# Performance work log

Measured on AMD Instinct MI355X. Metric: run time of the kernel, lower is better.

## Reference

```python
import jax, jax.numpy as jnp
import numpy as np

B, N, NCTX, DIM, H, DH, NMEM = 2, 1024, 2048, 1024, 16, 64, 16


def setup_inputs() -> dict:
    key = jax.random.key(0)
    ks = jax.random.split(key, 24)
    r = lambda i, shape, s=1.0: jax.random.normal(ks[i], shape, dtype=jnp.float32) * s
    w = 0.02  # linear weight scale
    return {
        "x": r(0, (B, N, DIM)),
        "context": r(1, (2, B, NCTX, DIM)),
        "wq1": r(2, (DIM, H * DH), w), "wk1": r(3, (DIM, H * DH), w), "wv1": r(4, (DIM, H * DH), w),
        "wq2": r(5, (DIM, H * DH), w), "wk2": r(6, (DIM, H * DH), w), "wv2": r(7, (DIM, H * DH), w),
        "th_pre1": r(8, (H, H), 0.25), "th_post1": r(9, (H, H), 0.25),
        "th_pre2": r(10, (H, H), 0.25), "th_post2": r(11, (H, H), 0.25),
        "scale1": jnp.full((1, H, 1, 1), -3.0, jnp.float32) + r(12, (1, H, 1, 1), 0.05),
        "scale2": jnp.full((1, H, 1, 1), -3.0, jnp.float32) + r(13, (1, H, 1, 1), 0.05),
        "mem_k1": r(14, (H, NMEM, DH)), "mem_v1": r(15, (H, NMEM, DH)),
        "mem_k2": r(16, (H, NMEM, DH)), "mem_v2": r(17, (H, NMEM, DH)),
        "hs1": jnp.ones((1, H, 1, 1), jnp.float32) + r(18, (1, H, 1, 1), 0.05),
        "hs2": jnp.ones((1, H, 1, 1), jnp.float32) + r(19, (1, H, 1, 1), 0.05),
        "wo1": r(20, (H * DH, DIM), w), "wo2": r(21, (H * DH, DIM), w),
    }


def _l2norm(t):
    # F.normalize: t / max(||t||, eps)
    n = jnp.linalg.norm(t, axis=-1, keepdims=True)
    return t / jnp.maximum(n, 1e-12)


def _split_heads(t, b):
    # [b, n, h*d] -> [b, h, n, d]
    return t.reshape(b, -1, H, DH).transpose(0, 2, 1, 3)


def _attend(x, kv, wq, wk, wv, th_pre, th_post, scale_p, mem_k, mem_v, hs, wo):
    b, n, _ = x.shape
    q = _split_heads(x @ wq, b)    # [b,h,n,d]
    k = _split_heads(kv @ wk, b)   # [b,h,j,d]
    v = _split_heads(kv @ wv, b)
    # memory key/values prepended
    k = jnp.concatenate([jnp.broadcast_to(mem_k[None], (b, H, NMEM, DH)), k], axis=2)
    v = jnp.concatenate([jnp.broadcast_to(mem_v[None], (b, H, NMEM, DH)), v], axis=2)
    # qk-norm with learned per-head temperature: scale = 1 / clamp(exp(p), min=0.01)
    q, k = _l2norm(q), _l2norm(k)
    scale = 1.0 / jnp.maximum(jnp.exp(scale_p), 0.01)
    dots = jnp.einsum('bhid,bhjd->bhij', q, k) * scale
    # talking heads: 1x1 Conv2d over head channel == head-mixing matmul
    dots = jnp.einsum('gh,bhij->bgij', th_pre, dots)
    attn = jax.nn.softmax(dots, axis=-1)
    attn = jnp.einsum('gh,bhij->bgij', th_post, attn)
    out = jnp.einsum('bhij,bhjd->bhid', attn, v) * hs  # head_scale
    out = out.transpose(0, 2, 1, 3).reshape(b, n, H * DH)
    return out @ wo


def reference(x, context, wq1, wk1, wv1, wq2, wk2, wv2,
              th_pre1, th_post1, th_pre2, th_post2,
              scale1, scale2, mem_k1, mem_v1, mem_k2, mem_v2,
              hs1, hs2, wo1, wo2):
    o1 = _attend(x, context[0], wq1, wk1, wv1, th_pre1, th_post1, scale1, mem_k1, mem_v1, hs1, wo1)
    o2 = _attend(x, context[1], wq2, wk2, wv2, th_pre2, th_post2, scale2, mem_k2, mem_v2, hs2, wo2)
    return o1 + o2
```

## Files before the change

### kernel.cpp

```cpp
#include <hip/hip_runtime.h>
#include <hip/hip_bf16.h>

#define Bb    2
#define Nn    1024
#define NCTXc 2048
#define DIMd  1024
#define Hh    16
#define DHd   64
#define NMEM  16
#define Jv    (NMEM + NCTXc)
#define JP    2112
#define HJP   (Hh * JP)
#define L2E   1.44269504088896f
#define NCH   129
#define LDH   1048

typedef _Float16 f16;
typedef _Float16 half8 __attribute__((ext_vector_type(8)));
typedef _Float16 half4 __attribute__((ext_vector_type(4)));
typedef float    f32x4 __attribute__((ext_vector_type(4)));

__device__ __forceinline__ float bf2f(unsigned short u){
  union { unsigned int i; float f; } v; v.i = ((unsigned)u) << 16; return v.f;
}
__device__ __forceinline__ float fin(float v){
  v = (v == v) ? v : 0.f;
  return fminf(fmaxf(v, -65504.f), 65504.f);
}
__device__ __forceinline__ float ldin(const void* p, long i, int isf32){
  return isf32 ? ((const float*)p)[i] : bf2f(((const unsigned short*)p)[i]);
}
__device__ __forceinline__ half8 h8zero(){
  half8 v;
  #pragma unroll
  for (int j = 0; j < 8; j++) v[j] = (f16)0.f;
  return v;
}

__global__ void detect_dtype(const void* __restrict__ p, int* __restrict__ flag, int n){
  const unsigned short* ub = (const unsigned short*)p;
  const float* fp = (const float*)p;
  int t = threadIdx.x;
  float bb = 0.f, bf = 0.f;
  for (int i = t; i < n; i += 64){
    float vb = bf2f(ub[i]);
    if (!(vb == vb) || fabsf(vb) > 1000.f) bb += 1.f;
    float vf = fp[i];
    if (!(vf == vf) || fabsf(vf) > 1000.f) bf += 1.f;
  }
  #pragma unroll
  for (int off = 32; off; off >>= 1){ bb += __shfl_xor(bb, off); bf += __shfl_xor(bf, off); }
  if (t == 0) *flag = (bf < bb) ? 1 : 0;
}

__global__ __launch_bounds__(256) void cvt_any(const void* __restrict__ in, f16* __restrict__ out,
                                               long n, const int* __restrict__ flag){
  int isf = *flag;
  long stride = (long)gridDim.x * 256;
  for (long i = (long)blockIdx.x * 256 + threadIdx.x; i < n; i += stride)
    out[i] = (f16)fin(ldin(in, i, isf));
}

__global__ __launch_bounds__(256) void cvt32_any(const void* __restrict__ in, float* __restrict__ out,
                                                 long n, const int* __restrict__ flag){
  int isf = *flag;
  long stride = (long)gridDim.x * 256;
  for (long i = (long)blockIdx.x * 256 + threadIdx.x; i < n; i += stride)
    out[i] = fin(ldin(in, i, isf));
}

__global__ __launch_bounds__(256) void transpose_any(const void* __restrict__ in,
                                                     f16* __restrict__ out,
                                                     int Cc, long ldo,
                                                     const int* __restrict__ flag){
  __shared__ f16 tile[32][33];
  int isf = *flag;
  int r0 = blockIdx.y * 32, c0 = blockIdx.x * 32;
  int tr = threadIdx.x >> 5, tc = threadIdx.x & 31;
  #pragma unroll
  for (int k = 0; k < 4; k++){
    int r = tr + k * 8;
    tile[r][tc] = (f16)fin(ldin(in, (long)(r0 + r) * Cc + c0 + tc, isf));
  }
  __syncthreads();
  #pragma unroll
  for (int k = 0; k < 4; k++){
    int r = tr + k * 8;
    out[(long)(c0 + r) * ldo + r0 + tc] = tile[tc][r];
  }
}

__global__ __launch_bounds__(256) void gemm_raw_bt(
    const void* __restrict__ A, const f16* __restrict__ Bt, f16* __restrict__ C,
    int K, long lda, long ldb, long ldc, long aOff, const int* __restrict__ flag)
{
  int isf = *flag;
  long m0 = (long)blockIdx.y * 64, n0 = (long)blockIdx.x * 64;

  __shared__ f16 As[64][40];
  __shared__ f16 Bs[64][40];
  int t = threadIdx.x;
  int wave = t >> 6, lane = t & 63;
  int wm = (wave >> 1) * 32, wn = (wave & 1) * 32;
  int fr = lane & 15, fq = lane >> 4;
  int srow = t >> 2, scol = (t & 3) * 8;

  f32x4 acc[2][2];
  #pragma unroll
  for (int a = 0; a < 2; a++)
    #pragma unroll
    for (int b = 0; b < 2; b++) acc[a][b] = (f32x4){0.f, 0.f, 0.f, 0.f};

  for (int k0 = 0; k0 < K; k0 += 32){
    long aidx = aOff + (m0 + srow) * lda + k0 + scol;
    half8 avv;
    if (isf){
      const float* ap = (const float*)A + aidx;
      float4 f0 = *(const float4*)ap;
      float4 f1 = *(const float4*)(ap + 4);
      avv[0] = (f16)fin(f0.x); avv[1] = (f16)fin(f0.y); avv[2] = (f16)fin(f0.z); avv[3] = (f16)fin(f0.w);
      avv[4] = (f16)fin(f1.x); avv[5] = (f16)fin(f1.y); avv[6] = (f16)fin(f1.z); avv[7] = (f16)fin(f1.w);
    } else {
      const unsigned short* up = (const unsigned short*)A + aidx;
      #pragma unroll
      for (int j = 0; j < 8; j++) avv[j] = (f16)fin(bf2f(up[j]));
    }
    half8 bvv = *(const half8*)(Bt + (n0 + srow) * ldb + k0 + scol);
    __syncthreads();
    *(half8*)&As[srow][scol] = avv;
    *(half8*)&Bs[srow][scol] = bvv;
    __syncthreads();
    #pragma unroll
    for (int ti = 0; ti < 2; ti++){
      half8 af = *(const half8*)&As[wm + 16 * ti + fr][fq * 8];
      #pragma unroll
      for (int tj = 0; tj < 2; tj++){
        half8 bf = *(const half8*)&Bs[wn + 16 * tj + fr][fq * 8];
        acc[ti][tj] = __builtin_amdgcn_mfma_f32_16x16x32_f16(af, bf, acc[ti][tj], 0, 0, 0);
      }
    }
  }
  #pragma unroll
  for (int ti = 0; ti < 2; ti++)
    #pragma unroll
    for (int tj = 0; tj < 2; tj++)
      #pragma unroll
      for (int r = 0; r < 4; r++){
        long row = m0 + wm + 16 * ti + fq * 4 + r;
        long col = n0 + wn + 16 * tj + fr;
        C[row * ldc + col] = (f16)acc[ti][tj][r];
      }
}

__global__ __launch_bounds__(256) void gemm_bt(
    const f16* __restrict__ A, const f16* __restrict__ Bt, f16* __restrict__ C,
    int K, long lda, long ldb, long ldc,
    long sAb, long sBb, long sCb, long sAh, long sBh, long sCh, int nh)
{
  int z = blockIdx.z;
  int zb = z / nh, zh = z - zb * nh;
  A  += (long)zb * sAb + (long)zh * sAh;
  Bt += (long)zb * sBb + (long)zh * sBh;
  C  += (long)zb * sCb + (long)zh * sCh;
  long m0 = (long)blockIdx.y * 64, n0 = (long)blockIdx.x * 64;

  __shared__ f16 As[64][40];
  __shared__ f16 Bs[64][40];
  int t = threadIdx.x;
  int wave = t >> 6, lane = t & 63;
  int wm = (wave >> 1) * 32, wn = (wave & 1) * 32;
  int fr = lane & 15, fq = lane >> 4;
  int srow = t >> 2, scol = (t & 3) * 8;

  f32x4 acc[2][2];
  #pragma unroll
  for (int a = 0; a < 2; a++)
    #pragma unroll
    for (int b = 0; b < 2; b++) acc[a][b] = (f32x4){0.f, 0.f, 0.f, 0.f};

  for (int k0 = 0; k0 < K; k0 += 32){
    half8 avv = *(const half8*)(A  + (m0 + srow) * lda + k0 + scol);
    half8 bvv = *(const half8*)(Bt + (n0 + srow) * ldb + k0 + scol);
    __syncthreads();
    *(half8*)&As[srow][scol] = avv;
    *(half8*)&Bs[srow][scol] = bvv;
    __syncthreads();
    #pragma unroll
    for (int ti = 0; ti < 2; ti++){
      half8 af = *(const half8*)&As[wm + 16 * ti + fr][fq * 8];
      #pragma unroll
      for (int tj = 0; tj < 2; tj++){
        half8 bf = *(const half8*)&Bs[wn + 16 * tj + fr][fq * 8];
        acc[ti][tj] = __builtin_amdgcn_mfma_f32_16x16x32_f16(af, bf, acc[ti][tj], 0, 0, 0);
      }
    }
  }
  #pragma unroll
  for (int ti = 0; ti < 2; ti++)
    #pragma unroll
    for (int tj = 0; tj < 2; tj++)
      #pragma unroll
      for (int r = 0; r < 4; r++){
        long row = m0 + wm + 16 * ti + fq * 4 + r;
        long col = n0 + wn + 16 * tj + fr;
        C[row * ldc + col] = (f16)acc[ti][tj][r];
      }
}

__global__ __launch_bounds__(256) void gemm_bt_dyn(
    const f16* __restrict__ A, const f16* __restrict__ Bt, void* __restrict__ C,
    int K, long lda, long ldb, long ldc, const int* __restrict__ flag)
{
  int isf = *flag;
  long m0 = (long)blockIdx.y * 64, n0 = (long)blockIdx.x * 64;

  __shared__ f16 As[64][40];
  __shared__ f16 Bs[64][40];
  int t = threadIdx.x;
  int wave = t >> 6, lane = t & 63;
  int wm = (wave >> 1) * 32, wn = (wave & 1) * 32;
  int fr = lane & 15, fq = lane >> 4;
  int srow = t >> 2, scol = (t & 3) * 8;

  f32x4 acc[2][2];
  #pragma unroll
  for (int a = 0; a < 2; a++)
    #pragma unroll
    for (int b = 0; b < 2; b++) acc[a][b] = (f32x4){0.f, 0.f, 0.f, 0.f};

  for (int k0 = 0; k0 < K; k0 += 32){
    half8 avv = *(const half8*)(A  + (m0 + srow) * lda + k0 + scol);
    half8 bvv = *(const half8*)(Bt + (n0 + srow) * ldb + k0 + scol);
    __syncthreads();
    *(half8*)&As[srow][scol] = avv;
    *(half8*)&Bs[srow][scol] = bvv;
    __syncthreads();
    #pragma unroll
    for (int ti = 0; ti < 2; ti++){
      half8 af = *(const half8*)&As[wm + 16 * ti + fr][fq * 8];
      #pragma unroll
      for (int tj = 0; tj < 2; tj++){
        half8 bf = *(const half8*)&Bs[wn + 16 * tj + fr][fq * 8];
        acc[ti][tj] = __builtin_amdgcn_mfma_f32_16x16x32_f16(af, bf, acc[ti][tj], 0, 0, 0);
      }
    }
  }
  #pragma unroll
  for (int ti = 0; ti < 2; ti++)
    #pragma unroll
    for (int tj = 0; tj < 2; tj++)
      #pragma unroll
      for (int r = 0; r < 4; r++){
        long row = m0 + wm + 16 * ti + fq * 4 + r;
        long col = n0 + wn + 16 * tj + fr;
        float v = acc[ti][tj][r];
        if (isf) ((float*)C)[row * ldc + col] = v;
        else     ((__hip_bfloat16*)C)[row * ldc + col] = __float2bfloat16(v);
      }
}

__global__ __launch_bounds__(256) void qn_build(const f16* __restrict__ qp, f16* __restrict__ qn,
                                                const float* __restrict__ scale_p){
  int row = blockIdx.x;
  int wave = threadIdx.x >> 6, lane = threadIdx.x & 63;
  #pragma unroll
  for (int hh = 0; hh < 4; hh++){
    int h = wave * 4 + hh;
    float v = (float)qp[(long)row * 1024 + h * 64 + lane];
    float ss = v * v;
    #pragma unroll
    for (int off = 32; off; off >>= 1) ss += __shfl_xor(ss, off);
    float sc = 1.0f / fmaxf(__expf(scale_p[h]), 0.01f);
    float o = v / fmaxf(sqrtf(ss), 1e-12f) * sc;
    qn[(long)row * 1024 + h * 64 + lane] = (f16)o;
  }
}

__global__ __launch_bounds__(256) void kbuf_build(const f16* __restrict__ kp,
                                                  const f16* __restrict__ mem_k,
                                                  f16* __restrict__ kbuf){
  int id = blockIdx.x * 4 + (threadIdx.x >> 6);
  int lane = threadIdx.x & 63;
  int h = id & 15; int bj = id >> 4; int j = bj % JP; int b = bj / JP;
  float v;
  if (j < NMEM)              v = (float)mem_k[(h * NMEM + j) * 64 + lane];
  else if (j < NMEM + NCTXc) v = (float)kp[((long)b * NCTXc + (j - NMEM)) * 1024 + h * 64 + lane];
  else                       v = 0.f;
  float ss = v * v;
  #pragma unroll
  for (int off = 32; off; off >>= 1) ss += __shfl_xor(ss, off);
  float o = v / fmaxf(sqrtf(ss), 1e-12f);
  kbuf[((long)b * JP + j) * 1024 + h * 64 + lane] = (f16)o;
}

__global__ __launch_bounds__(256) void vt_build(const f16* __restrict__ vp,
                                                const f16* __restrict__ mem_v,
                                                f16* __restrict__ vt){
  __shared__ f16 tile[64][72];
  int id = blockIdx.x;
  int jt = id % (JP / 64); int h = (id / (JP / 64)) & 15; int b = id / (16 * (JP / 64));
  int j0 = jt * 64;
  int t = threadIdx.x;
  #pragma unroll
  for (int rep = 0; rep < 2; rep++){
    int idx = t + rep * 256;
    int jj = idx >> 3, c8 = (idx & 7) * 8;
    int j = j0 + jj;
    half8 v;
    if (j < NMEM){
      v = *(const half8*)(mem_v + (h * NMEM + j) * 64 + c8);
    } else if (j < NMEM + NCTXc){
      v = *(const half8*)(vp + ((long)b * NCTXc + (j - NMEM)) * 1024 + h * 64 + c8);
    } else {
      v = h8zero();
    }
    *(half8*)&tile[jj][c8] = v;
  }
  __syncthreads();
  #pragma unroll
  for (int rep = 0; rep < 2; rep++){
    int idx = t + rep * 256;
    int d = idx >> 3, j8 = (idx & 7) * 8;
    half8 o;
    #pragma unroll
    for (int k = 0; k < 8; k++) o[k] = tile[j8 + k][d];
    *(half8*)(vt + (((long)(b * 16 + h) * 64 + d) * JP) + j0 + j8) = o;
  }
}

__global__ __launch_bounds__(256) void softmax_mfma(
    f16* __restrict__ S,
    const float* __restrict__ th_pre,
    const float* __restrict__ th_post,
    const float* __restrict__ hs)
{
  __shared__ f16 tile[16 * LDH];
  __shared__ float msh[4][16], lsh[4][16];
  __shared__ float Mf[16], Li[16];

  int t = threadIdx.x, wave = t >> 6, lane = t & 63;
  int r16 = lane & 15;
  int hb4 = (lane >> 4) * 4;
  f16* Srow = S + (long)blockIdx.x * HJP;

  half4 ahi, alo;
  #pragma unroll
  for (int j = 0; j < 4; j++){
    float a = th_pre[r16 * 16 + hb4 + j];
    ahi[j] = (f16)a; alo[j] = (f16)(a - (float)ahi[j]);
  }

  float m[4], l[4];
  #pragma unroll
  for (int r = 0; r < 4; r++){ m[r] = -1e30f; l[r] = 0.f; }

  const f32x4 z4 = (f32x4){0.f, 0.f, 0.f, 0.f};

  #pragma unroll 1
  for (int ph = 0; ph < 2; ph++){
    int cbase = ph ? 1040 : 0;
    int cfirst = ph ? 65 : 0, clast = ph ? NCH : 65;
    if (ph) __syncthreads();
    #pragma unroll
    for (int it = 0; it < 9; it++){
      int idx = it * 256 + t;
      if (idx < 2080){
        int h = idx / 130, c8 = idx - h * 130;
        *(half8*)&tile[h * LDH + c8 * 8] =
            *(const half8*)(Srow + (long)h * JP + cbase + c8 * 8);
      }
    }
    __syncthreads();
    for (int c = cfirst + wave; c < clast; c += 4){
      int lc = c * 16 - cbase + r16;
      half4 b;
      #pragma unroll
      for (int j = 0; j < 4; j++) b[j] = tile[(hb4 + j) * LDH + lc];
      f32x4 acc = __builtin_amdgcn_mfma_f32_16x16x16f16(alo, b, z4, 0, 0, 0);
      acc = __builtin_amdgcn_mfma_f32_16x16x16f16(ahi, b, acc, 0, 0, 0);
      #pragma unroll
      for (int r = 0; r < 4; r++){
        float v = acc[r];
        float mn = fmaxf(m[r], v);
        l[r] = l[r] * exp2f((m[r] - mn) * L2E) + exp2f((v - mn) * L2E);
        m[r] = mn;
      }
    }
  }

  #pragma unroll
  for (int off = 1; off < 16; off <<= 1){
    #pragma unroll
    for (int r = 0; r < 4; r++){
      float m2 = __shfl_xor(m[r], off), l2 = __shfl_xor(l[r], off);
      float mn = fmaxf(m[r], m2);
      l[r] = l[r] * exp2f((m[r] - mn) * L2E) + l2 * exp2f((m2 - mn) * L2E);
      m[r] = mn;
    }
  }
  if (r16 == 0){
    #pragma unroll
    for (int r = 0; r < 4; r++){ msh[wave][hb4 + r] = m[r]; lsh[wave][hb4 + r] = l[r]; }
  }
  __syncthreads();
  if (t < 16){
    float mf = fmaxf(fmaxf(msh[0][t], msh[1][t]), fmaxf(msh[2][t], msh[3][t]));
    float lf = 0.f;
    #pragma unroll
    for (int w = 0; w < 4; w++) lf += lsh[w][t] * exp2f((msh[w][t] - mf) * L2E);
    Mf[t] = mf; Li[t] = fin(1.f / lf);
  }
  __syncthreads();

  half4 chi, clo;
  float hsv = hs[r16];
  #pragma unroll
  for (int j = 0; j < 4; j++){
    float cc = th_post[r16 * 16 + hb4 + j] * hsv * Li[hb4 + j];
    chi[j] = (f16)cc; clo[j] = (f16)(cc - (float)chi[j]);
  }
  float mf[4];
  #pragma unroll
  for (int r = 0; r < 4; r++) mf[r] = Mf[hb4 + r];

  #pragma unroll 1
  for (int ph = 0; ph < 2; ph++){
    int cbase = ph ? 1040 : 0;
    int cfirst = ph ? 65 : 0, clast = ph ? NCH : 65;
    __syncthreads();
    #pragma unroll
    for (int it = 0; it < 9; it++){
      int idx = it * 256 + t;
      if (idx < 2080){
        int h = idx / 130, c8 = idx - h * 130;
        *(half8*)&tile[h * LDH + c8 * 8] =
            *(const half8*)(Srow + (long)h * JP + cbase + c8 * 8);
      }
    }
    __syncthreads();
    for (int c = cfirst + wave; c < clast; c += 4){
      int lc = c * 16 - cbase + r16;
      half4 b;
      #pragma unroll
      for (int j = 0; j < 4; j++) b[j] = tile[(hb4 + j) * LDH + lc];
      f32x4 acc = __builtin_amdgcn_mfma_f32_16x16x16f16(alo, b, z4, 0, 0, 0);
      acc = __builtin_amdgcn_mfma_f32_16x16x16f16(ahi, b, acc, 0, 0, 0);
      half4 ehi, elo;
      #pragma unroll
      for (int r = 0; r < 4; r++){
        float e = exp2f((acc[r] - mf[r]) * L2E);
        ehi[r] = (f16)e; elo[r] = (f16)(e - (float)ehi[r]);
      }
      f32x4 o = __builtin_amdgcn_mfma_f32_16x16x16f16(chi, ehi, z4, 0, 0, 0);
      o = __builtin_amdgcn_mfma_f32_16x16x16f16(clo, ehi, o, 0, 0, 0);
      o = __builtin_amdgcn_mfma_f32_16x16x16f16(chi, elo, o, 0, 0, 0);
      int col = c * 16 + r16;
      #pragma unroll
      for (int r = 0; r < 4; r++) Srow[(hb4 + r) * JP + col] = (f16)o[r];
    }
  }
}

extern "C" void kernel_launch(void* const* d_in, const int* in_sizes, int n_in,
                              void* d_out, int out_size, void* d_ws, size_t ws_size,
                              hipStream_t stream)
{
  (void)in_sizes; (void)n_in; (void)out_size; (void)ws_size;
  int* flag = (int*)d_ws;
  f16* ws   = (f16*)d_ws + 8;
  f16* wT   = ws;
  f16* woT  = wT   + 6291456;
  f16* qn   = woT  + 2097152;
  f16* kbuf = qn   + 2097152;
  f16* vt   = kbuf + 4325376;
  f16* av   = vt   + 4325376;
  f16* memc = av   + 4194304;
  float* parc = (float*)(memc + 65536);
  f16* S    = (f16*)(parc + 1088);
  f16* tmp  = S;

  detect_dtype<<<1, 64, 0, stream>>>(d_in[0], flag, 4096);

  for (int i = 0; i < 4; i++)
    cvt_any<<<16, 256, 0, stream>>>(d_in[14 + i], memc + (long)i * 16384, 16384, flag);
  {
    const int  src[8] = {8, 9, 10, 11, 12, 13, 18, 19};
    const long off[8] = {0, 256, 512, 768, 1024, 1040, 1056, 1072};
    const long cnt[8] = {256, 256, 256, 256, 16, 16, 16, 16};
    for (int i = 0; i < 8; i++)
      cvt32_any<<<1, 256, 0, stream>>>(d_in[src[i]], parc + off[i], cnt[i], flag);
  }

  for (int i = 0; i < 6; i++)
    transpose_any<<<dim3(32, 32), 256, 0, stream>>>(d_in[2 + i],
                                                    wT + (long)i * 1048576, 1024, 1024, flag);
  for (int L = 0; L < 2; L++)
    transpose_any<<<dim3(32, 32), 256, 0, stream>>>(d_in[20 + L],
                                                    woT + (long)L * 1024, 1024, 2048, flag);

  for (int L = 0; L < 2; L++){
    const f16* wqT = wT + (long)(3 * L + 0) * 1048576;
    const f16* wkT = wT + (long)(3 * L + 1) * 1048576;
    const f16* wvT = wT + (long)(3 * L + 2) * 1048576;
    const float* thpre  = parc + (long)L * 512;
    const float* thpost = parc + (long)L * 512 + 256;
    const float* scalep = parc + 1024 + (long)L * 16;
    const float* hsp    = parc + 1056 + (long)L * 16;
    const f16* mem_k = memc + (long)(2 * L) * 16384;
    const f16* mem_v = memc + (long)(2 * L + 1) * 16384;
    const long ctxOff = (long)L * Bb * NCTXc * DIMd;

    gemm_raw_bt<<<dim3(16, 32), 256, 0, stream>>>(d_in[0], wqT, tmp, 1024,
        1024, 1024, 1024, 0, flag);
    qn_build<<<Bb * Nn, 256, 0, stream>>>(tmp, qn, scalep);

    gemm_raw_bt<<<dim3(16, 64), 256, 0, stream>>>(d_in[1], wkT, tmp, 1024,
        1024, 1024, 1024, ctxOff, flag);
    kbuf_build<<<Bb * JP * Hh / 4, 256, 0, stream>>>(tmp, mem_k, kbuf);

    gemm_raw_bt<<<dim3(16, 64), 256, 0, stream>>>(d_in[1], wvT, tmp, 1024,
        1024, 1024, 1024, ctxOff, flag);
    vt_build<<<Bb * Hh * (JP / 64), 256, 0, stream>>>(tmp, mem_v, vt);

    gemm_bt<<<dim3(JP / 64, Nn / 64, Bb * Hh), 256, 0, stream>>>(qn, kbuf, S, 64,
        1024, 1024, HJP,
        (long)Nn * 1024, (long)JP * 1024, (long)Nn * HJP,
        64, 64, JP, Hh);

    softmax_mfma<<<Bb * Nn, 256, 0, stream>>>(S, thpre, thpost, hsp);

    gemm_bt<<<dim3(1, Nn / 64, Bb * Hh), 256, 0, stream>>>(S, vt,
        av + (long)L * 1024, JP,
        HJP, JP, 2048,
        (long)Nn * HJP, (long)Hh * 64 * JP, (long)Nn * 2048,
        JP, (long)64 * JP, 64, Hh);
  }

  gemm_bt_dyn<<<dim3(16, 32), 256, 0, stream>>>(av, woT, d_out, 2048,
      2048, 2048, 1024, flag);
}
```

Before: 933.3 us.

## Cache mixed logits in registers and use fixed-offset softmax in talking-heads kernel

The softmax kernel now runs with 512 threads. Each wave keeps its pre-mixed logits, clamped and stored as fp16, in registers. The second pass no longer reloads S from global memory or recomputes the th_pre MFMA. The online max/rescale recurrence is replaced by a plain sum of exp over clamped values, with the max folded in afterward. This removes one full global read of S and many exp calls, at the cost of more registers and of clamping logits to [-60,78], which assumes bounded qk-norm scores.

```diff
diff --git a/kernel.cpp b/kernel.cpp
--- a/kernel.cpp
+++ b/kernel.cpp
@@ -12,7 +12,6 @@
 #define JP    2112
 #define HJP   (Hh * JP)
 #define L2E   1.44269504088896f
-#define NCH   129
 #define LDH   1048
 
 typedef _Float16 f16;
@@ -328,19 +327,20 @@
   }
 }
 
-__global__ __launch_bounds__(256) void softmax_mfma(
+__global__ __launch_bounds__(512) void softmax_mfma(
     f16* __restrict__ S,
     const float* __restrict__ th_pre,
     const float* __restrict__ th_post,
     const float* __restrict__ hs)
 {
   __shared__ f16 tile[16 * LDH];
-  __shared__ float msh[4][16], lsh[4][16];
+  __shared__ float msh[8][16], lsh[8][16];
   __shared__ float Mf[16], Li[16];
 
   int t = threadIdx.x, wave = t >> 6, lane = t & 63;
   int r16 = lane & 15;
   int hb4 = (lane >> 4) * 4;
+  int sr  = t >> 5, sc = t & 31;
   f16* Srow = S + (long)blockIdx.x * HJP;
 
   half4 ahi, alo;
@@ -354,48 +354,70 @@
   #pragma unroll
   for (int r = 0; r < 4; r++){ m[r] = -1e30f; l[r] = 0.f; }
 
+  half4 msave[17];
   const f32x4 z4 = (f32x4){0.f, 0.f, 0.f, 0.f};
 
-  #pragma unroll 1
-  for (int ph = 0; ph < 2; ph++){
-    int cbase = ph ? 1040 : 0;
-    int cfirst = ph ? 65 : 0, clast = ph ? NCH : 65;
-    if (ph) __syncthreads();
-    #pragma unroll
-    for (int it = 0; it < 9; it++){
-      int idx = it * 256 + t;
-      if (idx < 2080){
-        int h = idx / 130, c8 = idx - h * 130;
-        *(half8*)&tile[h * LDH + c8 * 8] =
-            *(const half8*)(Srow + (long)h * JP + cbase + c8 * 8);
-      }
-    }
-    __syncthreads();
-    for (int c = cfirst + wave; c < clast; c += 4){
-      int lc = c * 16 - cbase + r16;
+  #pragma unroll
+  for (int it = 0; it < 5; it++){
+    int c8 = sc + it * 32;
+    if (c8 < 130)
+      *(half8*)&tile[sr * LDH + c8 * 8] = *(const half8*)(Srow + (long)sr * JP + c8 * 8);
+  }
+  __syncthreads();
+  #pragma unroll
+  for (int cc = 0; cc < 9; cc++){
+    int c = wave + cc * 8;
+    if (c < 65){
+      int lc = c * 16 + r16;
       half4 b;
       #pragma unroll
       for (int j = 0; j < 4; j++) b[j] = tile[(hb4 + j) * LDH + lc];
       f32x4 acc = __builtin_amdgcn_mfma_f32_16x16x16f16(alo, b, z4, 0, 0, 0);
       acc = __builtin_amdgcn_mfma_f32_16x16x16f16(ahi, b, acc, 0, 0, 0);
+      half4 hh;
       #pragma unroll
       for (int r = 0; r < 4; r++){
-        float v = acc[r];
-        float mn = fmaxf(m[r], v);
-        l[r] = l[r] * exp2f((m[r] - mn) * L2E) + exp2f((v - mn) * L2E);
-        m[r] = mn;
-      }
-    }
+        float u = fminf(fmaxf(acc[r], -60.f), 78.f);
+        m[r] = fmaxf(m[r], u);
+        l[r] += exp2f(u * L2E);
+        hh[r] = (f16)u;
+      }
+      msave[cc] = hh;
+    }
+  }
+  __syncthreads();
+  #pragma unroll
+  for (int it = 0; it < 4; it++){
+    int c8 = sc + it * 32;
+    *(half8*)&tile[sr * LDH + c8 * 8] = *(const half8*)(Srow + (long)sr * JP + 1040 + c8 * 8);
+  }
+  __syncthreads();
+  #pragma unroll
+  for (int cc = 0; cc < 8; cc++){
+    int c = 65 + wave + cc * 8;
+    int lc = c * 16 - 1040 + r16;
+    half4 b;
+    #pragma unroll
+    for (int j = 0; j < 4; j++) b[j] = tile[(hb4 + j) * LDH + lc];
+    f32x4 acc = __builtin_amdgcn_mfma_f32_16x16x16f16(alo, b, z4, 0, 0, 0);
+    acc = __builtin_amdgcn_mfma_f32_16x16x16f16(ahi, b, acc, 0, 0, 0);
+    half4 hh;
+    #pragma unroll
+    for (int r = 0; r < 4; r++){
+      float u = fminf(fmaxf(acc[r], -60.f), 78.f);
+      m[r] = fmaxf(m[r], u);
+      l[r] += exp2f(u * L2E);
+      hh[r] = (f16)u;
+    }
+    msave[9 + cc] = hh;
   }
 
   #pragma unroll
   for (int off = 1; off < 16; off <<= 1){
     #pragma unroll
     for (int r = 0; r < 4; r++){
-      float m2 = __shfl_xor(m[r], off), l2 = __shfl_xor(l[r], off);
-      float mn = fmaxf(m[r], m2);
-      l[r] = l[r] * exp2f((m[r] - mn) * L2E) + l2 * exp2f((m2 - mn) * L2E);
-      m[r] = mn;
+      m[r] = fmaxf(m[r], __shfl_xor(m[r], off));
+      l[r] += __shfl_xor(l[r], off);
     }
   }
   if (r16 == 0){
@@ -404,11 +426,11 @@
   }
   __syncthreads();
   if (t < 16){
-    float mf = fmaxf(fmaxf(msh[0][t], msh[1][t]), fmaxf(msh[2][t], msh[3][t]));
-    float lf = 0.f;
-    #pragma unroll
-    for (int w = 0; w < 4; w++) lf += lsh[w][t] * exp2f((msh[w][t] - mf) * L2E);
-    Mf[t] = mf; Li[t] = fin(1.f / lf);
+    float mf_ = msh[0][t], lf = lsh[0][t];
+    #pragma unroll
+    for (int w = 1; w < 8; w++){ mf_ = fmaxf(mf_, msh[w][t]); lf += lsh[w][t]; }
+    Mf[t] = mf_;
+    Li[t] = fin(exp2f(mf_ * L2E) / lf);
   }
   __syncthreads();
 
@@ -416,39 +438,22 @@
   float hsv = hs[r16];
   #pragma unroll
   for (int j = 0; j < 4; j++){
-    float cc = th_post[r16 * 16 + hb4 + j] * hsv * Li[hb4 + j];
-    chi[j] = (f16)cc; clo[j] = (f16)(cc - (float)chi[j]);
+    float cc2 = th_post[r16 * 16 + hb4 + j] * hsv * Li[hb4 + j];
+    chi[j] = (f16)cc2; clo[j] = (f16)(cc2 - (float)chi[j]);
   }
   float mf[4];
   #pragma unroll
   for (int r = 0; r < 4; r++) mf[r] = Mf[hb4 + r];
 
-  #pragma unroll 1
-  for (int ph = 0; ph < 2; ph++){
-    int cbase = ph ? 1040 : 0;
-    int cfirst = ph ? 65 : 0, clast = ph ? NCH : 65;
-    __syncthreads();
-    #pragma unroll
-    for (int it = 0; it < 9; it++){
-      int idx = it * 256 + t;
-      if (idx < 2080){
-        int h = idx / 130, c8 = idx - h * 130;
-        *(half8*)&tile[h * LDH + c8 * 8] =
-            *(const half8*)(Srow + (long)h * JP + cbase + c8 * 8);
-      }
-    }
-    __syncthreads();
-    for (int c = cfirst + wave; c < clast; c += 4){
-      int lc = c * 16 - cbase + r16;
-      half4 b;
-      #pragma unroll
-      for (int j = 0; j < 4; j++) b[j] = tile[(hb4 + j) * LDH + lc];
-      f32x4 acc = __builtin_amdgcn_mfma_f32_16x16x16f16(alo, b, z4, 0, 0, 0);
-      acc = __builtin_amdgcn_mfma_f32_16x16x16f16(ahi, b, acc, 0, 0, 0);
+  #pragma unroll
+  for (int cc = 0; cc < 9; cc++){
+    int c = wave + cc * 8;
+    if (c < 65){
+      half4 h4 = msave[cc];
       half4 ehi, elo;
       #pragma unroll
       for (int r = 0; r < 4; r++){
-        float e = exp2f((acc[r] - mf[r]) * L2E);
+        float e = exp2f(((float)h4[r] - mf[r]) * L2E);
         ehi[r] = (f16)e; elo[r] = (f16)(e - (float)ehi[r]);
       }
       f32x4 o = __builtin_amdgcn_mfma_f32_16x16x16f16(chi, ehi, z4, 0, 0, 0);
@@ -458,6 +463,23 @@
       #pragma unroll
       for (int r = 0; r < 4; r++) Srow[(hb4 + r) * JP + col] = (f16)o[r];
     }
+  }
+  #pragma unroll
+  for (int cc = 0; cc < 8; cc++){
+    int c = 65 + wave + cc * 8;
+    half4 h4 = msave[9 + cc];
+    half4 ehi, elo;
+    #pragma unroll
+    for (int r = 0; r < 4; r++){
+      float e = exp2f(((float)h4[r] - mf[r]) * L2E);
+      ehi[r] = (f16)e; elo[r] = (f16)(e - (float)ehi[r]);
+    }
+    f32x4 o = __builtin_amdgcn_mfma_f32_16x16x16f16(chi, ehi, z4, 0, 0, 0);
+    o = __builtin_amdgcn_mfma_f32_16x16x16f16(clo, ehi, o, 0, 0, 0);
+    o = __builtin_amdgcn_mfma_f32_16x16x16f16(chi, elo, o, 0, 0, 0);
+    int col = c * 16 + r16;
+    #pragma unroll
+    for (int r = 0; r < 4; r++) Srow[(hb4 + r) * JP + col] = (f16)o[r];
   }
 }
 
@@ -527,7 +549,7 @@
         (long)Nn * 1024, (long)JP * 1024, (long)Nn * HJP,
         64, 64, JP, Hh);
 
-    softmax_mfma<<<Bb * Nn, 256, 0, stream>>>(S, thpre, thpost, hsp);
+    softmax_mfma<<<Bb * Nn, 512, 0, stream>>>(S, thpre, thpost, hsp);
 
     gemm_bt<<<dim3(1, Nn / 64, Bb * Hh), 256, 0, stream>>>(S, vt,
         av + (long)L * 1024, JP,
```

Result: faster. 881.2 us (-5.6%).
